# Kernel tuning notes

Measured on AMD Instinct MI355X. Metric: run time of the kernel, lower is better.

Reference implementation:

```python
import jax, jax.numpy as jnp
import numpy as np

EPS = 1e-8  # torch F.cosine_similarity default eps


def setup_inputs() -> dict:
    key = jax.random.key(0)
    k1, k2, k3, k4 = jax.random.split(key, 4)
    B, S, D_in, D_e, E = 4, 128, 768, 256, 100000
    return {
        "x": jax.random.normal(k1, (B, S, D_in), dtype=jnp.float32),
        "W": jax.random.normal(k2, (D_e, D_in), dtype=jnp.float32) * 0.02,
        "b": jax.random.normal(k3, (D_e,), dtype=jnp.float32) * 0.02,
        "entity_embedding": jax.random.normal(k4, (E, D_e), dtype=jnp.float32),
    }


def reference(x, W, b, entity_embedding):
    # Linear projection + tanh: [B,S,D_e]
    q = jnp.tanh(jnp.einsum('bsi,ei->bse', x, W) + b)
    # Cosine similarity = L2-normalize both sides, then GEMM (fused; avoids
    # the [B,S,E,D] broadcast intermediate of the original).
    qn = q / jnp.maximum(jnp.linalg.norm(q, axis=-1, keepdims=True), EPS)
    en = entity_embedding / jnp.maximum(
        jnp.linalg.norm(entity_embedding, axis=-1, keepdims=True), EPS)
    return jnp.einsum('bsd,ed->bse', qn, en)  # [B,S,E]
```

## Files before the change

kernel.cpp:

```cpp
#include <hip/hip_runtime.h>
#include <hip/hip_bf16.h>

#define D_IN  768
#define D_E   256
#define M_TOT 512
#define E_TOT 100000

typedef __attribute__((ext_vector_type(4))) float f32x4;
typedef __attribute__((ext_vector_type(8))) short bf16x8;

__device__ __forceinline__ unsigned short bf16bits(float f) {
    union { __hip_bfloat16 h; unsigned short u; } c;
    c.h = __float2bfloat16(f);
    return c.u;
}

__device__ __forceinline__ void gload_lds16(const void* g, void* l) {
    __builtin_amdgcn_global_load_lds(
        (const __attribute__((address_space(1))) void*)g,
        (__attribute__((address_space(3))) void*)l, 16, 0, 0);
}

#define PROJ_BLOCKS 64
#define PREP_BLOCKS 1563
#define PP_GRID (PROJ_BLOCKS + PREP_BLOCKS)
#define PTM 8
#define PBK 64
#define PROUNDS (D_IN / PBK)

__global__ __launch_bounds__(512) void fused_pp(
    const float* __restrict__ x, const float* __restrict__ W,
    const float* __restrict__ b, const float* __restrict__ en,
    unsigned short* __restrict__ qb, unsigned short* __restrict__ eb)
{
    __shared__ float ws[D_E * (PBK + 1)];
    __shared__ float xs[PTM][PBK];
    __shared__ float red[PTM][4];
    __shared__ float qiv[PTM];

    const int t   = threadIdx.x;
    const int bid = blockIdx.x;

    if (bid >= PROJ_BLOCKS) {
        const int lane = t & 63;
        const int gw   = (bid - PROJ_BLOCKS) * 8 + (t >> 6);
        #pragma unroll 2
        for (int i = 0; i < 8; ++i) {
            const int row = gw * 8 + i;
            if (row >= E_TOT) break;
            const float4 v = *reinterpret_cast<const float4*>(
                en + (size_t)row * D_E + lane * 4);
            float s = v.x*v.x + v.y*v.y + v.z*v.z + v.w*v.w;
            #pragma unroll
            for (int off = 1; off < 64; off <<= 1) s += __shfl_xor(s, off, 64);
            const float sc = 1.0f / fmaxf(sqrtf(s), 1e-8f);
            union { unsigned short u[4]; uint2 d; } o;
            o.u[0] = bf16bits(v.x * sc); o.u[1] = bf16bits(v.y * sc);
            o.u[2] = bf16bits(v.z * sc); o.u[3] = bf16bits(v.w * sc);
            *reinterpret_cast<uint2*>(eb + (size_t)row * D_E + lane * 4) = o.d;
        }
        return;
    }

    const int m0   = bid * PTM;
    const int e    = t & 255;
    const int half = t >> 8;
    const int c4   = t & 15;
    const int rr   = t >> 4;

    float4 wreg[8];
    float  xreg = 0.f;
    float  acc[4] = {0.f, 0.f, 0.f, 0.f};

    #pragma unroll
    for (int i = 0; i < 8; ++i)
        wreg[i] = *reinterpret_cast<const float4*>(
            &W[(size_t)(i * 32 + rr) * D_IN + c4 * 4]);
    xreg = x[(size_t)(m0 + (t >> 6)) * D_IN + (t & 63)];

    for (int rd = 0; rd < PROUNDS; ++rd) {
        #pragma unroll
        for (int i = 0; i < 8; ++i) {
            float* dst = &ws[(i * 32 + rr) * (PBK + 1) + c4 * 4];
            dst[0] = wreg[i].x; dst[1] = wreg[i].y;
            dst[2] = wreg[i].z; dst[3] = wreg[i].w;
        }
        xs[t >> 6][t & 63] = xreg;
        __syncthreads();
        if (rd + 1 < PROUNDS) {
            const int k0 = (rd + 1) * PBK;
            #pragma unroll
            for (int i = 0; i < 8; ++i)
                wreg[i] = *reinterpret_cast<const float4*>(
                    &W[(size_t)(i * 32 + rr) * D_IN + k0 + c4 * 4]);
            xreg = x[(size_t)(m0 + (t >> 6)) * D_IN + k0 + (t & 63)];
        }
        #pragma unroll
        for (int k = 0; k < PBK; ++k) {
            const float wv = ws[e * (PBK + 1) + k];
            #pragma unroll
            for (int j = 0; j < 4; ++j)
                acc[j] = fmaf(xs[half * 4 + j][k], wv, acc[j]);
        }
        __syncthreads();
    }

    const float bias = b[e];
    const int wv4 = (t >> 6) & 3;
    const int lane = t & 63;
    float q[4];
    #pragma unroll
    for (int j = 0; j < 4; ++j) {
        q[j] = tanhf(acc[j] + bias);
        float s = q[j] * q[j];
        #pragma unroll
        for (int off = 1; off < 64; off <<= 1) s += __shfl_xor(s, off, 64);
        if (lane == 0) red[half * 4 + j][wv4] = s;
    }
    __syncthreads();
    if (t < PTM) {
        const float s = red[t][0] + red[t][1] + red[t][2] + red[t][3];
        qiv[t] = 1.0f / fmaxf(sqrtf(s), 1e-8f);
    }
    __syncthreads();
    #pragma unroll
    for (int j = 0; j < 4; ++j)
        qb[(size_t)(m0 + half * 4 + j) * D_E + e] =
            bf16bits(q[j] * qiv[half * 4 + j]);
}

#define BM 128
#define BN 64
#define TPB 25
#define NGRPN 63
#define SIM_GRID (NGRPN * (M_TOT / BM))

__global__ __launch_bounds__(512, 2) void sim_kernel(
    const unsigned short* __restrict__ eb, const unsigned short* __restrict__ qb,
    float* __restrict__ out)
{
    __shared__ unsigned short qs[BM * D_E];
    __shared__ unsigned short es[2][BN * D_E];

    const int t    = threadIdx.x;
    const int lane = t & 63;
    const int wid  = t >> 6;
    const int l15  = lane & 15;
    const int lk   = lane >> 4;
    const int wm   = (wid >> 1) * 32;
    const int wn   = (wid & 1) * 32;

    int vbid;
    {
        const int q = SIM_GRID >> 3, r = SIM_GRID & 7;
        const int xcd = blockIdx.x & 7, rk = blockIdx.x >> 3;
        vbid = (xcd < r ? xcd * (q + 1) : r * (q + 1) + (xcd - r) * q) + rk;
    }
    const int mg    = vbid & 3;
    const int ngrp  = vbid >> 2;
    const int m0    = mg * BM;
    const int nbase = ngrp * (TPB * BN);

    #pragma unroll
    for (int i = 0; i < 8; ++i) {
        const int c   = i * 512 + t;
        const int row = c >> 5;
        const int c16 = c & 31;
        const unsigned short* src =
            qb + (size_t)(m0 + row) * D_E + ((c16 ^ (row & 7)) << 3);
        gload_lds16(src, (void*)&qs[(size_t)c << 3]);
    }
    #pragma unroll
    for (int i = 0; i < 4; ++i) {
        const int c   = i * 512 + t;
        const int row = c >> 5;
        const int c16 = c & 31;
        int rg = nbase + row; if (rg >= E_TOT) rg = E_TOT - 1;
        const unsigned short* src =
            eb + (size_t)rg * D_E + ((c16 ^ (row & 7)) << 3);
        gload_lds16(src, (void*)&es[0][(size_t)c << 3]);
    }
    __syncthreads();

    const char* qsb = reinterpret_cast<const char*>(qs);

    for (int tt = 0; tt < TPB; ++tt) {
        const int n0 = nbase + tt * BN;
        if (n0 >= E_TOT) break;
        const int cur = tt & 1;

        const int nn0 = n0 + BN;
        if (tt + 1 < TPB && nn0 < E_TOT) {
            #pragma unroll
            for (int i = 0; i < 4; ++i) {
                const int c   = i * 512 + t;
                const int row = c >> 5;
                const int c16 = c & 31;
                int rg = nn0 + row; if (rg >= E_TOT) rg = E_TOT - 1;
                const unsigned short* src =
                    eb + (size_t)rg * D_E + ((c16 ^ (row & 7)) << 3);
                gload_lds16(src, (void*)&es[cur ^ 1][(size_t)c << 3]);
            }
        }

        const char* esb = reinterpret_cast<const char*>(&es[cur][0]);

        f32x4 acc[2][2];
        #pragma unroll
        for (int mf = 0; mf < 2; ++mf)
            #pragma unroll
            for (int nf = 0; nf < 2; ++nf)
                acc[mf][nf] = (f32x4){0.f, 0.f, 0.f, 0.f};

        #pragma unroll
        for (int ks = 0; ks < 8; ++ks) {
            const int kb = ks * 64 + lk * 16;
            bf16x8 ef[2];
            #pragma unroll
            for (int nf = 0; nf < 2; ++nf) {
                const int row = wn + nf * 16 + l15;
                const int cb  = kb ^ ((row & 7) << 4);
                ef[nf] = *reinterpret_cast<const bf16x8*>(esb + row * 512 + cb);
            }
            #pragma unroll
            for (int mf = 0; mf < 2; ++mf) {
                const int rq  = wm + mf * 16 + l15;
                const int cbq = kb ^ ((rq & 7) << 4);
                const bf16x8 qf =
                    *reinterpret_cast<const bf16x8*>(qsb + rq * 512 + cbq);
                acc[mf][0] = __builtin_amdgcn_mfma_f32_16x16x32_bf16(
                    ef[0], qf, acc[mf][0], 0, 0, 0);
                acc[mf][1] = __builtin_amdgcn_mfma_f32_16x16x32_bf16(
                    ef[1], qf, acc[mf][1], 0, 0, 0);
            }
        }

        __syncthreads();

        #pragma unroll
        for (int mf = 0; mf < 2; ++mf) {
            const int m = m0 + wm + mf * 16 + l15;
            #pragma unroll
            for (int nf = 0; nf < 2; ++nf) {
                const int n = n0 + wn + nf * 16 + lk * 4;
                if (n < E_TOT)
                    *reinterpret_cast<f32x4*>(&out[(size_t)m * E_TOT + n]) =
                        acc[mf][nf];
            }
        }
    }
}

extern "C" void kernel_launch(void* const* d_in, const int* in_sizes, int n_in,
                              void* d_out, int out_size, void* d_ws, size_t ws_size,
                              hipStream_t stream) {
    const float* x  = (const float*)d_in[0];
    const float* W  = (const float*)d_in[1];
    const float* b  = (const float*)d_in[2];
    const float* en = (const float*)d_in[3];
    float* out = (float*)d_out;

    unsigned short* qb = (unsigned short*)d_ws;
    unsigned short* eb = (unsigned short*)((char*)d_ws + (size_t)M_TOT * D_E * 2);

    fused_pp<<<PP_GRID, 512, 0, stream>>>(x, W, b, en, qb, eb);
    sim_kernel<<<SIM_GRID, 512, 0, stream>>>(eb, qb, out);
}
```

Before: 141.5 us.

## Drop LDS staging in sim kernel; keep Q fragments in registers and prefetch E

The similarity kernel no longer stages operands through shared memory. Each wave holds its Q fragments in registers for the whole block and loads entity fragments straight from global memory into registers, split into two K-halves so the next tile loads while MFMAs run on the current one. Blocks shrink to 256 threads covering 64 rows, with 3 blocks per CU and MFMA priority raised through s_setprio. This removes LDS traffic and block-wide barriers. In exchange, each E row is fetched by more blocks (8 M-groups instead of 4), global loads are less coalesced, and register pressure rises.

```diff
diff --git a/kernel.cpp b/kernel.cpp
--- a/kernel.cpp
+++ b/kernel.cpp
@@ -13,12 +13,6 @@
     union { __hip_bfloat16 h; unsigned short u; } c;
     c.h = __float2bfloat16(f);
     return c.u;
-}
-
-__device__ __forceinline__ void gload_lds16(const void* g, void* l) {
-    __builtin_amdgcn_global_load_lds(
-        (const __attribute__((address_space(1))) void*)g,
-        (__attribute__((address_space(3))) void*)l, 16, 0, 0);
 }
 
 #define PROJ_BLOCKS 64
@@ -129,19 +123,18 @@
             bf16bits(q[j] * qiv[half * 4 + j]);
 }
 
-#define BM 128
-#define BN 64
 #define TPB 25
 #define NGRPN 63
-#define SIM_GRID (NGRPN * (M_TOT / BM))
-
-__global__ __launch_bounds__(512, 2) void sim_kernel(
+#define SIM_GRID (8 * NGRPN)
+
+__device__ __forceinline__ f32x4 mfma16(bf16x8 a, bf16x8 b, f32x4 c) {
+    return __builtin_amdgcn_mfma_f32_16x16x32_bf16(a, b, c, 0, 0, 0);
+}
+
+__global__ __launch_bounds__(256, 3) void sim_kernel(
     const unsigned short* __restrict__ eb, const unsigned short* __restrict__ qb,
     float* __restrict__ out)
 {
-    __shared__ unsigned short qs[BM * D_E];
-    __shared__ unsigned short es[2][BN * D_E];
-
     const int t    = threadIdx.x;
     const int lane = t & 63;
     const int wid  = t >> 6;
@@ -150,61 +143,43 @@
     const int wm   = (wid >> 1) * 32;
     const int wn   = (wid & 1) * 32;
 
-    int vbid;
-    {
-        const int q = SIM_GRID >> 3, r = SIM_GRID & 7;
-        const int xcd = blockIdx.x & 7, rk = blockIdx.x >> 3;
-        vbid = (xcd < r ? xcd * (q + 1) : r * (q + 1) + (xcd - r) * q) + rk;
-    }
-    const int mg    = vbid & 3;
-    const int ngrp  = vbid >> 2;
-    const int m0    = mg * BM;
-    const int nbase = ngrp * (TPB * BN);
-
-    #pragma unroll
-    for (int i = 0; i < 8; ++i) {
-        const int c   = i * 512 + t;
-        const int row = c >> 5;
-        const int c16 = c & 31;
-        const unsigned short* src =
-            qb + (size_t)(m0 + row) * D_E + ((c16 ^ (row & 7)) << 3);
-        gload_lds16(src, (void*)&qs[(size_t)c << 3]);
-    }
-    #pragma unroll
-    for (int i = 0; i < 4; ++i) {
-        const int c   = i * 512 + t;
-        const int row = c >> 5;
-        const int c16 = c & 31;
-        int rg = nbase + row; if (rg >= E_TOT) rg = E_TOT - 1;
-        const unsigned short* src =
-            eb + (size_t)rg * D_E + ((c16 ^ (row & 7)) << 3);
-        gload_lds16(src, (void*)&es[0][(size_t)c << 3]);
-    }
-    __syncthreads();
-
-    const char* qsb = reinterpret_cast<const char*>(qs);
+    const int vbid  = (blockIdx.x & 7) * NGRPN + (blockIdx.x >> 3);
+    const int mg    = vbid & 7;
+    const int ngrp  = vbid >> 3;
+    const int m0    = mg * 64;
+    const int nbase = ngrp * (TPB * 64);
+
+    bf16x8 qf[2][8];
+    #pragma unroll
+    for (int mf = 0; mf < 2; ++mf)
+        #pragma unroll
+        for (int ks = 0; ks < 8; ++ks)
+            qf[mf][ks] = *reinterpret_cast<const bf16x8*>(
+                qb + (size_t)(m0 + wm + mf * 16 + l15) * D_E + ks * 32 + lk * 8);
+    #pragma unroll
+    for (int mf = 0; mf < 2; ++mf)
+        #pragma unroll
+        for (int ks = 0; ks < 8; ++ks)
+            asm volatile("" : "+v"(qf[mf][ks]));
+
+    const unsigned short* ebl = eb + (size_t)lk * 8;
+    #define EADDR(tt, nf) ({                                                  \
+        int n_ = nbase + (tt) * 64 + wn + (nf) * 16 + l15;                    \
+        if (n_ >= E_TOT) n_ = E_TOT - 1;                                      \
+        ebl + (size_t)n_ * D_E; })
+
+    bf16x8 ca[2][4], cb[2][4];
+    #pragma unroll
+    for (int nf = 0; nf < 2; ++nf) {
+        const unsigned short* p = EADDR(0, nf);
+        #pragma unroll
+        for (int kk = 0; kk < 4; ++kk) {
+            ca[nf][kk] = *reinterpret_cast<const bf16x8*>(p + kk * 32);
+            cb[nf][kk] = *reinterpret_cast<const bf16x8*>(p + 128 + kk * 32);
+        }
+    }
 
     for (int tt = 0; tt < TPB; ++tt) {
-        const int n0 = nbase + tt * BN;
-        if (n0 >= E_TOT) break;
-        const int cur = tt & 1;
-
-        const int nn0 = n0 + BN;
-        if (tt + 1 < TPB && nn0 < E_TOT) {
-            #pragma unroll
-            for (int i = 0; i < 4; ++i) {
-                const int c   = i * 512 + t;
-                const int row = c >> 5;
-                const int c16 = c & 31;
-                int rg = nn0 + row; if (rg >= E_TOT) rg = E_TOT - 1;
-                const unsigned short* src =
-                    eb + (size_t)rg * D_E + ((c16 ^ (row & 7)) << 3);
-                gload_lds16(src, (void*)&es[cur ^ 1][(size_t)c << 3]);
-            }
-        }
-
-        const char* esb = reinterpret_cast<const char*>(&es[cur][0]);
-
         f32x4 acc[2][2];
         #pragma unroll
         for (int mf = 0; mf < 2; ++mf)
@@ -212,43 +187,60 @@
             for (int nf = 0; nf < 2; ++nf)
                 acc[mf][nf] = (f32x4){0.f, 0.f, 0.f, 0.f};
 
-        #pragma unroll
-        for (int ks = 0; ks < 8; ++ks) {
-            const int kb = ks * 64 + lk * 16;
-            bf16x8 ef[2];
+        __builtin_amdgcn_s_setprio(1);
+        #pragma unroll
+        for (int kk = 0; kk < 4; ++kk)
+            #pragma unroll
+            for (int mf = 0; mf < 2; ++mf) {
+                acc[mf][0] = mfma16(ca[0][kk], qf[mf][kk], acc[mf][0]);
+                acc[mf][1] = mfma16(ca[1][kk], qf[mf][kk], acc[mf][1]);
+            }
+        __builtin_amdgcn_s_setprio(0);
+
+        if (tt + 1 < TPB) {
             #pragma unroll
             for (int nf = 0; nf < 2; ++nf) {
-                const int row = wn + nf * 16 + l15;
-                const int cb  = kb ^ ((row & 7) << 4);
-                ef[nf] = *reinterpret_cast<const bf16x8*>(esb + row * 512 + cb);
-            }
+                const unsigned short* p = EADDR(tt + 1, nf);
+                #pragma unroll
+                for (int kk = 0; kk < 4; ++kk)
+                    ca[nf][kk] = *reinterpret_cast<const bf16x8*>(p + kk * 32);
+            }
+        }
+
+        __builtin_amdgcn_s_setprio(1);
+        #pragma unroll
+        for (int kk = 0; kk < 4; ++kk)
             #pragma unroll
             for (int mf = 0; mf < 2; ++mf) {
-                const int rq  = wm + mf * 16 + l15;
-                const int cbq = kb ^ ((rq & 7) << 4);
-                const bf16x8 qf =
-                    *reinterpret_cast<const bf16x8*>(qsb + rq * 512 + cbq);
-                acc[mf][0] = __builtin_amdgcn_mfma_f32_16x16x32_bf16(
-                    ef[0], qf, acc[mf][0], 0, 0, 0);
-                acc[mf][1] = __builtin_amdgcn_mfma_f32_16x16x32_bf16(
-                    ef[1], qf, acc[mf][1], 0, 0, 0);
-            }
-        }
-
-        __syncthreads();
-
+                acc[mf][0] = mfma16(cb[0][kk], qf[mf][kk + 4], acc[mf][0]);
+                acc[mf][1] = mfma16(cb[1][kk], qf[mf][kk + 4], acc[mf][1]);
+            }
+        __builtin_amdgcn_s_setprio(0);
+
+        if (tt + 1 < TPB) {
+            #pragma unroll
+            for (int nf = 0; nf < 2; ++nf) {
+                const unsigned short* p = EADDR(tt + 1, nf);
+                #pragma unroll
+                for (int kk = 0; kk < 4; ++kk)
+                    cb[nf][kk] = *reinterpret_cast<const bf16x8*>(p + 128 + kk * 32);
+            }
+        }
+
+        const int n0t = nbase + tt * 64;
         #pragma unroll
         for (int mf = 0; mf < 2; ++mf) {
             const int m = m0 + wm + mf * 16 + l15;
             #pragma unroll
             for (int nf = 0; nf < 2; ++nf) {
-                const int n = n0 + wn + nf * 16 + lk * 4;
+                const int n = n0t + wn + nf * 16 + lk * 4;
                 if (n < E_TOT)
                     *reinterpret_cast<f32x4*>(&out[(size_t)m * E_TOT + n]) =
                         acc[mf][nf];
             }
         }
     }
+    #undef EADDR
 }
 
 extern "C" void kernel_launch(void* const* d_in, const int* in_sizes, int n_in,
@@ -264,5 +256,5 @@
     unsigned short* eb = (unsigned short*)((char*)d_ws + (size_t)M_TOT * D_E * 2);
 
     fused_pp<<<PP_GRID, 512, 0, stream>>>(x, W, b, en, qb, eb);
-    sim_kernel<<<SIM_GRID, 512, 0, stream>>>(eb, qb, out);
-}
+    sim_kernel<<<SIM_GRID, 256, 0, stream>>>(eb, qb, out);
+}
```

New measurement: 177.9 us. 25.8% more time.
